# Kernel optimization log

Measured on AMD Instinct MI355X. Metric: run time of the kernel, lower is better.

The kernel has to match this reference:

```python
import jax, jax.numpy as jnp
import numpy as np

B, S, D, H = 4, 1024, 1024, 16
HD = D // H
MAX_DIST, WIN, MAX_SPAN = 512, 256, 512
TEMP_SCALE = 0.01
EPS = 1e-5


def _ln(x, g, b):
    m = x.mean(-1, keepdims=True)
    v = ((x - m) ** 2).mean(-1, keepdims=True)
    return (x - m) * jax.lax.rsqrt(v + EPS) * g + b


def _heads(t):
    b, s, _ = t.shape
    return t.reshape(b, s, H, HD).transpose(0, 2, 1, 3)


def _merge(t):
    b, _, s, _ = t.shape
    return t.transpose(0, 2, 1, 3).reshape(b, s, D)


def _global_attn(x, Wq, bq, Wk, Wv, bv, Wo, bo):
    # MultiheadC with mask tensor passed -> is_causal=True SDPA (default 1/sqrt(HD) scale)
    q = _heads(x @ Wq.T + bq)
    k = _heads(x @ Wk.T)
    v = _heads(x @ Wv.T + bv)
    s = jnp.einsum('bhqd,bhkd->bhqk', q, k) / float(np.sqrt(HD))
    n = x.shape[1]
    causal = jnp.tril(jnp.ones((n, n), bool))
    s = jnp.where(causal, s, jnp.finfo(s.dtype).min)
    w = jax.nn.softmax(s, axis=-1)
    return _merge(jnp.einsum('bhqk,bhkd->bhqd', w, v)) @ Wo.T + bo


def _span_attn(q, k, v, temp):
    # AdaptiveSpan core: softmax(QK^T / temperature * head_dim**-0.25) V
    scale = HD ** -0.25
    qh, kh, vh = _heads(q), _heads(k), _heads(v)
    w = jax.nn.softmax(jnp.einsum('bhqd,bhkd->bhqk', qh, kh) / temp * scale, axis=-1)
    return _merge(jnp.einsum('bhqk,bhkd->bhqd', w, vh))


def _slide_win(local, span_mean, win, span_len, local_max):
    bx, sx, dx = local.shape
    temp = 1.0 + TEMP_SCALE * (1.0 - span_mean)  # sharpen=True branch
    outs = []
    for st in range(0, sx, win):  # static unrolled loop over windows (ragged slices)
        en = min(st + win, sx)
        wlen = en - st
        ks = max(0, st - span_len + win)
        ke = min(st + span_len, sx)
        klen = ke - ks
        eff = min(int(wlen * span_mean), wlen, klen, local_max)
        if eff <= 0:
            outs.append(jnp.zeros((bx, wlen, dx), local.dtype))
            continue
        o = _span_attn(local[:, st:st + eff], local[:, ks:ks + eff], local[:, ks:ks + eff], temp)
        if eff < wlen:
            o = jnp.concatenate([o, jnp.zeros((bx, wlen - eff, dx), local.dtype)], axis=1)
        outs.append(o)
    return jnp.concatenate(outs, axis=1)


def setup_inputs() -> dict:
    key = jax.random.key(0)
    ks = jax.random.split(key, 8)
    qkv_std = 1.0 / float(np.sqrt(HD))
    return {
        'x': jax.random.normal(ks[0], (B, S, D), jnp.float32),
        'ln_a_g': jnp.ones((D,), jnp.float32),
        'ln_a_b': jnp.zeros((D,), jnp.float32),
        'ln_b_g': jnp.ones((D,), jnp.float32),
        'ln_b_b': jnp.zeros((D,), jnp.float32),
        'Wq': jax.random.normal(ks[1], (D, D), jnp.float32) * qkv_std,
        'bq': jnp.zeros((D,), jnp.float32),
        'Wk': jax.random.normal(ks[2], (D, D), jnp.float32) * qkv_std,
        'Wv': jax.random.normal(ks[3], (D, D), jnp.float32) * qkv_std,
        'bv': jnp.zeros((D,), jnp.float32),
        'Wo': jax.random.normal(ks[4], (D, D), jnp.float32) * 0.02,
        'bo': jnp.zeros((D,), jnp.float32),
        'Wp': jax.random.normal(ks[5], (1, D), jnp.float32) * float(np.sqrt(2.0 / (D + 1))),
        'bp': jnp.zeros((1,), jnp.float32),
        'Wproj': jax.random.normal(ks[6], (D, 2 * D), jnp.float32) * 0.02,
        'bproj': jnp.zeros((D,), jnp.float32),
    }


def reference(x, ln_a_g, ln_a_b, ln_b_g, ln_b_b, Wq, bq, Wk, Wv, bv, Wo, bo, Wp, bp, Wproj, bproj):
    local = _ln(x, ln_a_g, ln_a_b)
    globe = _ln(x, ln_b_g, ln_b_b)
    globe_out = _global_attn(globe, Wq, bq, Wk, Wv, bv, Wo, bo)
    # Predictor: sigmoid(Linear(mean over seq))
    base_scale = jax.nn.sigmoid(globe_out.mean(axis=1) @ Wp.T + bp)  # [B, 1]
    span_scale = jnp.clip(base_scale, 0.0, 1.0)  # RL refine factor fixed at 1.0 (deterministic)
    span_mean = float(jnp.mean(span_scale))  # mirrors torch .item() host sync
    win = max(1, int(WIN * span_mean))
    span_len = max(1, int(MAX_SPAN * span_mean))
    local_max = min(MAX_DIST, span_len, win)
    local_out = _slide_win(local, span_mean, win, span_len, local_max)
    combined = jnp.concatenate([local_out, globe_out], axis=-1)
    return combined @ Wproj.T + bproj
```

## Files before the change

### kernel.cpp

```cpp
#include <hip/hip_runtime.h>
#include <math.h>

#define B_ 4
#define S_ 1024
#define D_ 1024
#define H_ 16
#define HD_ 64
#define BSD_ (B_*S_*D_)

using short8 = __attribute__((ext_vector_type(8))) short;
using f32x4  = __attribute__((ext_vector_type(4))) float;

#define MFMA16(a,b,c) __builtin_amdgcn_mfma_f32_16x16x32_bf16((a),(b),(c),0,0,0)

__device__ __forceinline__ ushort f2bf(float f) {
  uint u = __float_as_uint(f);
  return (ushort)((u + 0x7fffu + ((u >> 16) & 1u)) >> 16);
}
__device__ __forceinline__ float bf2f(ushort h) {
  return __uint_as_float(((uint)h) << 16);
}
__device__ __forceinline__ void split8(const float* p, short8* hi, short8* lo) {
  #pragma unroll
  for (int j = 0; j < 8; j++) {
    ushort h = f2bf(p[j]);
    (*hi)[j] = (short)h;
    (*lo)[j] = (short)f2bf(p[j] - bf2f(h));
  }
}
__device__ __forceinline__ void async_load16(const ushort* g, ushort* l) {
  __builtin_amdgcn_global_load_lds(
      (const __attribute__((address_space(1))) unsigned int*)g,
      (__attribute__((address_space(3))) unsigned int*)l, 16, 0, 0);
}

__device__ __forceinline__ float block_reduce_sum_256(float v, float* sbuf) {
  #pragma unroll
  for (int off = 32; off > 0; off >>= 1) v += __shfl_xor(v, off, 64);
  int lane = threadIdx.x & 63, wid = threadIdx.x >> 6;
  __syncthreads();
  if (lane == 0) sbuf[wid] = v;
  __syncthreads();
  return sbuf[0] + sbuf[1] + sbuf[2] + sbuf[3];
}

__global__ __launch_bounds__(256) void ln_kernel(const float* __restrict__ x,
                                                 const float* __restrict__ g,
                                                 const float* __restrict__ bta,
                                                 float* __restrict__ out) {
  __shared__ float sbuf[4];
  const int row = blockIdx.x;
  const float* xr = x + (size_t)row * D_;
  const int t = threadIdx.x;
  float v[4]; float s = 0.f;
  #pragma unroll
  for (int i = 0; i < 4; i++) { v[i] = xr[t + 256*i]; s += v[i]; }
  const float mean = block_reduce_sum_256(s, sbuf) * (1.0f/D_);
  float sq = 0.f;
  #pragma unroll
  for (int i = 0; i < 4; i++) { float d = v[i]-mean; sq += d*d; }
  const float var = block_reduce_sum_256(sq, sbuf) * (1.0f/D_);
  const float r = rsqrtf(var + 1e-5f);
  float* orow = out + (size_t)row * D_;
  #pragma unroll
  for (int i = 0; i < 4; i++) {
    int c = t + 256*i;
    orow[c] = (v[i]-mean)*r*g[c] + bta[c];
  }
}

__global__ __launch_bounds__(256) void ln_split_kernel(const float* __restrict__ x,
                                                       const float* __restrict__ g,
                                                       const float* __restrict__ bta,
                                                       ushort* __restrict__ out) {
  __shared__ float sbuf[4];
  const int row = blockIdx.x;
  const int t = threadIdx.x;
  const int c = t*4;
  const float* xr = x + (size_t)row * D_;
  float4 v = *(const float4*)(xr + c);
  float s = v.x + v.y + v.z + v.w;
  const float mean = block_reduce_sum_256(s, sbuf) * (1.0f/D_);
  float4 dv = make_float4(v.x-mean, v.y-mean, v.z-mean, v.w-mean);
  float sq = dv.x*dv.x + dv.y*dv.y + dv.z*dv.z + dv.w*dv.w;
  const float var = block_reduce_sum_256(sq, sbuf) * (1.0f/D_);
  const float r = rsqrtf(var + 1e-5f);
  float4 gg = *(const float4*)(g + c);
  float4 bb = *(const float4*)(bta + c);
  float n[4];
  n[0] = dv.x*r*gg.x + bb.x; n[1] = dv.y*r*gg.y + bb.y;
  n[2] = dv.z*r*gg.z + bb.z; n[3] = dv.w*r*gg.w + bb.w;
  ushort4 hi, lo;
  hi.x = f2bf(n[0]); hi.y = f2bf(n[1]); hi.z = f2bf(n[2]); hi.w = f2bf(n[3]);
  lo.x = f2bf(n[0]-bf2f(hi.x)); lo.y = f2bf(n[1]-bf2f(hi.y));
  lo.z = f2bf(n[2]-bf2f(hi.z)); lo.w = f2bf(n[3]-bf2f(hi.w));
  ushort* orow = out + (size_t)row*2048;
  *(ushort4*)(orow + c)        = hi;
  *(ushort4*)(orow + 1024 + c) = lo;
}

__global__ __launch_bounds__(256) void split_w3_kernel(const float* __restrict__ Wq,
                                                       const float* __restrict__ Wk,
                                                       const float* __restrict__ Wv,
                                                       const float* __restrict__ bq,
                                                       const float* __restrict__ bv,
                                                       ushort* __restrict__ out,
                                                       float* __restrict__ biascat) {
  const int idx = blockIdx.x*256 + threadIdx.x;
  const int n = idx >> 8;
  const int col4 = (idx & 255) << 2;
  const float* src = (n < 1024) ? (Wq + (size_t)n*1024)
                   : (n < 2048) ? (Wk + (size_t)(n-1024)*1024)
                                : (Wv + (size_t)(n-2048)*1024);
  const float4 a = *(const float4*)(src + col4);
  ushort4 hi, lo;
  hi.x = f2bf(a.x); hi.y = f2bf(a.y); hi.z = f2bf(a.z); hi.w = f2bf(a.w);
  lo.x = f2bf(a.x - bf2f(hi.x)); lo.y = f2bf(a.y - bf2f(hi.y));
  lo.z = f2bf(a.z - bf2f(hi.z)); lo.w = f2bf(a.w - bf2f(hi.w));
  ushort* orow = out + (size_t)n*2048;
  *(ushort4*)(orow + col4)        = hi;
  *(ushort4*)(orow + 1024 + col4) = lo;
  if (idx < 3072)
    biascat[idx] = (idx < 1024) ? bq[idx] : (idx < 2048) ? 0.f : bv[idx-2048];
}

__global__ __launch_bounds__(256) void split_w1_kernel(const float* __restrict__ W,
                                                       ushort* __restrict__ out) {
  const int idx = blockIdx.x*256 + threadIdx.x;
  const int n = idx >> 8;
  const int col4 = (idx & 255) << 2;
  const float4 a = *(const float4*)(W + (size_t)n*1024 + col4);
  ushort4 hi, lo;
  hi.x = f2bf(a.x); hi.y = f2bf(a.y); hi.z = f2bf(a.z); hi.w = f2bf(a.w);
  lo.x = f2bf(a.x - bf2f(hi.x)); lo.y = f2bf(a.y - bf2f(hi.y));
  lo.z = f2bf(a.z - bf2f(hi.z)); lo.w = f2bf(a.w - bf2f(hi.w));
  ushort* orow = out + (size_t)n*2048;
  *(ushort4*)(orow + col4)        = hi;
  *(ushort4*)(orow + 1024 + col4) = lo;
}

__global__ __launch_bounds__(256) void cvt_bf16_kernel(const float* __restrict__ in,
                                                       ushort* __restrict__ out,
                                                       int gprshift, int ostride, int ooff) {
  const int idx = blockIdx.x*256 + threadIdx.x;
  const int row = idx >> gprshift;
  const int col4 = (idx & ((1 << gprshift) - 1)) << 2;
  const int ncols = 4 << gprshift;
  const float4 a = *(const float4*)(in + (size_t)row*ncols + col4);
  ushort4 hi;
  hi.x = f2bf(a.x); hi.y = f2bf(a.y); hi.z = f2bf(a.z); hi.w = f2bf(a.w);
  *(ushort4*)(out + (size_t)row*ostride + ooff + col4) = hi;
}

__global__ __launch_bounds__(256) void mfma_gemm_qkv(
    const ushort* __restrict__ A, const ushort* __restrict__ Bw,
    const float* __restrict__ bias,
    ushort* __restrict__ Qsp, ushort* __restrict__ Ksp,
    ushort* __restrict__ Vth, ushort* __restrict__ Vtl, int Kh) {
  __shared__ __align__(16) ushort smem[17408];
  ushort* Ash = smem;
  ushort* Asl = smem + 4096;
  ushort* Bsh = smem + 8192;
  ushort* Bsl = smem + 12288;
  const int lda = 2*Kh;
  const int tid = threadIdx.x;
  const int bm = blockIdx.y * 128, bn = blockIdx.x * 128;
  const int wave = tid >> 6, lane = tid & 63;
  const int wm = wave >> 1, wn = wave & 1;
  const int lm = lane & 15, q = lane >> 4;
  const int lrow = lane >> 2;
  const int sw = (((lane & 3) ^ ((lane >> 3) & 3)) << 3);

  f32x4 acc[4][4];
  #pragma unroll
  for (int i = 0; i < 4; i++)
    #pragma unroll
    for (int j = 0; j < 4; j++)
      acc[i][j] = (f32x4){0.f,0.f,0.f,0.f};

  const ushort* Agh = A  + (size_t)(bm + wave*32 + lrow)*lda + sw;
  const ushort* Agl = Agh + Kh;
  const ushort* Bgh = Bw + (size_t)(bn + wave*32 + lrow)*lda + sw;
  const ushort* Bgl = Bgh + Kh;
  const size_t r16a = (size_t)16*lda;
  ushort* AhD0 = &Ash[(wave*32)*32];      ushort* AhD1 = &Ash[(wave*32+16)*32];
  ushort* AlD0 = &Asl[(wave*32)*32];      ushort* AlD1 = &Asl[(wave*32+16)*32];
  ushort* BhD0 = &Bsh[(wave*32)*32];      ushort* BhD1 = &Bsh[(wave*32+16)*32];
  ushort* BlD0 = &Bsl[(wave*32)*32];      ushort* BlD1 = &Bsl[(wave*32+16)*32];
  const int rsw  = ((q ^ ((lm >> 1) & 3)) << 3);
  const int aoff = (wm*64 + lm)*32 + rsw;
  const int boff = (wn*64 + lm)*32 + rsw;

  for (int k0 = 0; k0 < Kh; k0 += 32) {
    __syncthreads();
    async_load16(Agh + k0, AhD0);
    async_load16(Agh + r16a + k0, AhD1);
    async_load16(Agl + k0, AlD0);
    async_load16(Agl + r16a + k0, AlD1);
    async_load16(Bgh + k0, BhD0);
    async_load16(Bgh + r16a + k0, BhD1);
    async_load16(Bgl + k0, BlD0);
    async_load16(Bgl + r16a + k0, BlD1);
    __syncthreads();
    short8 ah[4], al[4], bh[4], bl[4];
    #pragma unroll
    for (int mt = 0; mt < 4; mt++) {
      ah[mt] = *(const short8*)&Ash[aoff + mt*512];
      al[mt] = *(const short8*)&Asl[aoff + mt*512];
    }
    #pragma unroll
    for (int nt = 0; nt < 4; nt++) {
      bh[nt] = *(const short8*)&Bsh[boff + nt*512];
      bl[nt] = *(const short8*)&Bsl[boff + nt*512];
    }
    #pragma unroll
    for (int mt = 0; mt < 4; mt++)
      #pragma unroll
      for (int nt = 0; nt < 4; nt++) {
        f32x4 a = acc[mt][nt];
        a = MFMA16(ah[mt], bh[nt], a);
        a = MFMA16(al[mt], bh[nt], a);
        a = MFMA16(ah[mt], bl[nt], a);
        acc[mt][nt] = a;
      }
  }

  const int b = bm >> 10, s0 = bm & 1023;
  if (blockIdx.x < 16) {
    ushort* dst = (blockIdx.x < 8) ? Qsp : Ksp;
    const int h = ((bn + wn*64) >> 6) & 15;
    #pragma unroll
    for (int mt = 0; mt < 4; mt++) {
      #pragma unroll
      for (int nt = 0; nt < 4; nt++) {
        const int n = bn + wn*64 + nt*16 + lm;
        const int d = nt*16 + lm;
        const float bb = bias[n];
        #pragma unroll
        for (int reg = 0; reg < 4; reg++) {
          const int s = s0 + wm*64 + mt*16 + q*4 + reg;
          const float val = acc[mt][nt][reg] + bb;
          const ushort hi = f2bf(val);
          const ushort lo = f2bf(val - bf2f(hi));
          ushort* rp = dst + ((size_t)((b*16 + h)*1024 + s))*128;
          rp[d] = hi; rp[64 + d] = lo;
        }
      }
    }
  } else {
    ushort* Th = smem;
    ushort* Tl = smem + 8704;
    #pragma unroll
    for (int c = 0; c < 2; c++) {
      __syncthreads();
      if (wn == c) {
        #pragma unroll
        for (int mt = 0; mt < 4; mt++)
          #pragma unroll
          for (int nt = 0; nt < 4; nt++) {
            const int nl = nt*16 + lm;
            const float bb = bias[bn + c*64 + nl];
            #pragma unroll
            for (int reg = 0; reg < 4; reg++) {
              const int sl = wm*64 + mt*16 + q*4 + reg;
              const float val = acc[mt][nt][reg] + bb;
              const ushort hi = f2bf(val);
              const ushort lo = f2bf(val - bf2f(hi));
              Th[nl*136 + sl] = hi;
              Tl[nl*136 + sl] = lo;
            }
          }
      }
      __syncthreads();
      const int nl = tid >> 2, s32 = (tid & 3)*32;
      const int h = ((bn - 2048 + c*64) >> 6) & 15;
      const size_t drow = ((size_t)((b*16 + h)*64 + nl))*1024 + s0 + s32;
      #pragma unroll
      for (int j = 0; j < 4; j++) {
        *(short8*)(Vth + drow + j*8) = *(const short8*)&Th[nl*136 + s32 + j*8];
        *(short8*)(Vtl + drow + j*8) = *(const short8*)&Tl[nl*136 + s32 + j*8];
      }
    }
  }
}

__global__ __launch_bounds__(256) void mfma_gemm2(
    const ushort* __restrict__ A, const ushort* __restrict__ Bw,
    const float* __restrict__ bias, float* __restrict__ C,
    int Kh, int ldc, ushort* __restrict__ aux) {
  __shared__ __align__(16) ushort Ash[128*32];
  __shared__ __align__(16) ushort Asl[128*32];
  __shared__ __align__(16) ushort Bsh[128*32];
  __shared__ __align__(16) ushort Bsl[128*32];
  const int lda = 2*Kh;
  const int tid = threadIdx.x;
  const int bm = blockIdx.y * 128, bn = blockIdx.x * 128;
  const int wave = tid >> 6, lane = tid & 63;
  const int wm = wave >> 1, wn = wave & 1;
  const int lm = lane & 15, q = lane >> 4;
  const int lrow = lane >> 2;
  const int sw = (((lane & 3) ^ ((lane >> 3) & 3)) << 3);

  f32x4 acc[4][4];
  #pragma unroll
  for (int i = 0; i < 4; i++)
    #pragma unroll
    for (int j = 0; j < 4; j++)
      acc[i][j] = (f32x4){0.f,0.f,0.f,0.f};

  const ushort* Agh = A  + (size_t)(bm + wave*32 + lrow)*lda + sw;
  const ushort* Agl = Agh + Kh;
  const ushort* Bgh = Bw + (size_t)(bn + wave*32 + lrow)*lda + sw;
  const ushort* Bgl = Bgh + Kh;
  const size_t r16a = (size_t)16*lda;
  ushort* AhD0 = &Ash[(wave*32)*32];      ushort* AhD1 = &Ash[(wave*32+16)*32];
  ushort* AlD0 = &Asl[(wave*32)*32];      ushort* AlD1 = &Asl[(wave*32+16)*32];
  ushort* BhD0 = &Bsh[(wave*32)*32];      ushort* BhD1 = &Bsh[(wave*32+16)*32];
  ushort* BlD0 = &Bsl[(wave*32)*32];      ushort* BlD1 = &Bsl[(wave*32+16)*32];
  const int rsw  = ((q ^ ((lm >> 1) & 3)) << 3);
  const int aoff = (wm*64 + lm)*32 + rsw;
  const int boff = (wn*64 + lm)*32 + rsw;

  for (int k0 = 0; k0 < Kh; k0 += 32) {
    __syncthreads();
    async_load16(Agh + k0, AhD0);
    async_load16(Agh + r16a + k0, AhD1);
    async_load16(Agl + k0, AlD0);
    async_load16(Agl + r16a + k0, AlD1);
    async_load16(Bgh + k0, BhD0);
    async_load16(Bgh + r16a + k0, BhD1);
    async_load16(Bgl + k0, BlD0);
    async_load16(Bgl + r16a + k0, BlD1);
    __syncthreads();
    short8 ah[4], al[4], bh[4], bl[4];
    #pragma unroll
    for (int mt = 0; mt < 4; mt++) {
      ah[mt] = *(const short8*)&Ash[aoff + mt*512];
      al[mt] = *(const short8*)&Asl[aoff + mt*512];
    }
    #pragma unroll
    for (int nt = 0; nt < 4; nt++) {
      bh[nt] = *(const short8*)&Bsh[boff + nt*512];
      bl[nt] = *(const short8*)&Bsl[boff + nt*512];
    }
    #pragma unroll
    for (int mt = 0; mt < 4; mt++)
      #pragma unroll
      for (int nt = 0; nt < 4; nt++) {
        f32x4 a = acc[mt][nt];
        a = MFMA16(ah[mt], bh[nt], a);
        a = MFMA16(al[mt], bh[nt], a);
        a = MFMA16(ah[mt], bl[nt], a);
        acc[mt][nt] = a;
      }
  }

  #pragma unroll
  for (int mt = 0; mt < 4; mt++) {
    #pragma unroll
    for (int nt = 0; nt < 4; nt++) {
      const int n = bn + wn*64 + nt*16 + lm;
      const float bb = bias ? bias[n] : 0.f;
      #pragma unroll
      for (int reg = 0; reg < 4; reg++) {
        const int m = bm + wm*64 + mt*16 + q*4 + reg;
        const float val = acc[mt][nt][reg] + bb;
        C[(size_t)m*ldc + n] = val;
        if (aux) aux[(size_t)m*2048 + 1024 + n] = f2bf(val);
      }
    }
  }
}

__global__ __launch_bounds__(256) void mfma_gemm(
    const ushort* __restrict__ A, const ushort* __restrict__ Bw,
    const float* __restrict__ bias, float* __restrict__ C,
    int K, int ldc) {
  __shared__ __align__(16) ushort As[128*32];
  __shared__ __align__(16) ushort Bs[128*32];
  const int tid = threadIdx.x;
  const int bm = blockIdx.y * 128, bn = blockIdx.x * 128;
  const int wave = tid >> 6, lane = tid & 63;
  const int wm = wave >> 1, wn = wave & 1;
  const int lm = lane & 15, q = lane >> 4;
  const int lrow = lane >> 2;
  const int sw = (((lane & 3) ^ ((lane >> 3) & 3)) << 3);

  f32x4 acc[4][4];
  #pragma unroll
  for (int i = 0; i < 4; i++)
    #pragma unroll
    for (int j = 0; j < 4; j++)
      acc[i][j] = (f32x4){0.f,0.f,0.f,0.f};

  const ushort* Ar0 = A  + (size_t)(bm + wave*32 + lrow)*K + sw;
  const ushort* Br0 = Bw + (size_t)(bn + wave*32 + lrow)*K + sw;
  const size_t r16 = (size_t)16*K;
  ushort* AsD0 = &As[(wave*32)*32];
  ushort* AsD1 = &As[(wave*32 + 16)*32];
  ushort* BsD0 = &Bs[(wave*32)*32];
  ushort* BsD1 = &Bs[(wave*32 + 16)*32];
  const int rsw  = ((q ^ ((lm >> 1) & 3)) << 3);
  const int aoff0 = (wm*64 + lm)*32 + rsw;
  const int boff0 = (wn*64 + lm)*32 + rsw;

  for (int k0 = 0; k0 < K; k0 += 32) {
    __syncthreads();
    async_load16(Ar0 + k0, AsD0);
    async_load16(Ar0 + r16 + k0, AsD1);
    async_load16(Br0 + k0, BsD0);
    async_load16(Br0 + r16 + k0, BsD1);
    __syncthreads();
    short8 af[4], bf[4];
    #pragma unroll
    for (int mt = 0; mt < 4; mt++) af[mt] = *(const short8*)&As[aoff0 + mt*512];
    #pragma unroll
    for (int nt = 0; nt < 4; nt++) bf[nt] = *(const short8*)&Bs[boff0 + nt*512];
    #pragma unroll
    for (int mt = 0; mt < 4; mt++)
      #pragma unroll
      for (int nt = 0; nt < 4; nt++)
        acc[mt][nt] = MFMA16(af[mt], bf[nt], acc[mt][nt]);
  }

  #pragma unroll
  for (int mt = 0; mt < 4; mt++) {
    #pragma unroll
    for (int nt = 0; nt < 4; nt++) {
      const int n = bn + wn*64 + nt*16 + lm;
      const float bb = bias ? bias[n] : 0.f;
      #pragma unroll
      for (int reg = 0; reg < 4; reg++) {
        const int m = bm + wm*64 + mt*16 + q*4 + reg;
        C[(size_t)m*ldc + n] = acc[mt][nt][reg] + bb;
      }
    }
  }
}

__device__ __forceinline__ void attn_unit(
    int qt, int kt, int w, int lm, int q,
    const short8 qh[2], const short8 ql[2],
    const ushort* Kc, const ushort* Vc, float* Pf,
    f32x4 of[4], float mst[4], float lst[4]) {
  f32x4 sS[4];
  #pragma unroll
  for (int nt = 0; nt < 4; nt++) {
    const ushort* kr = &Kc[(nt*16 + lm)*136 + q*8];
    const short8 kh0 = *(const short8*)(kr);
    const short8 kh1 = *(const short8*)(kr + 32);
    const short8 kl0 = *(const short8*)(kr + 64);
    const short8 kl1 = *(const short8*)(kr + 96);
    f32x4 a = (f32x4){0.f,0.f,0.f,0.f};
    a = MFMA16(qh[0], kh0, a);
    a = MFMA16(ql[0], kh0, a);
    a = MFMA16(qh[0], kl0, a);
    a = MFMA16(qh[1], kh1, a);
    a = MFMA16(ql[1], kh1, a);
    a = MFMA16(qh[1], kl1, a);
    sS[nt] = a;
  }
  const int ktbase = kt*64;
  const int qrow0 = qt*64 + w*16 + q*4;
  #pragma unroll
  for (int rm = 0; rm < 4; rm++) {
    const int qrow = qrow0 + rm;
    float v[4];
    #pragma unroll
    for (int nt = 0; nt < 4; nt++) {
      const int kcol = ktbase + nt*16 + lm;
      const float x = sS[nt][rm]*0.125f;
      v[nt] = (kcol <= qrow) ? x : -INFINITY;
    }
    float tm = fmaxf(fmaxf(v[0],v[1]), fmaxf(v[2],v[3]));
    #pragma unroll
    for (int off = 1; off < 16; off <<= 1) tm = fmaxf(tm, __shfl_xor(tm, off, 64));
    const float nm = fmaxf(mst[rm], tm);
    const float alpha = __expf(mst[rm] - nm);
    float ps = 0.f;
    #pragma unroll
    for (int nt = 0; nt < 4; nt++) {
      float p = __expf(v[nt] - nm);
      sS[nt][rm] = p;
      ps += p;
    }
    #pragma unroll
    for (int off = 1; off < 16; off <<= 1) ps += __shfl_xor(ps, off, 64);
    lst[rm] = lst[rm]*alpha + ps;
    mst[rm] = nm;
    #pragma unroll
    for (int nt = 0; nt < 4; nt++) of[nt][rm] *= alpha;
  }
  #pragma unroll
  for (int rm = 0; rm < 4; rm++)
    #pragma unroll
    for (int nt = 0; nt < 4; nt++)
      Pf[(w*16 + q*4 + rm)*66 + nt*16 + lm] = sS[nt][rm];
  short8 ph[2], pl[2];
  {
    const float* prow = &Pf[(w*16 + lm)*66];
    float pv[16];
    *(float4*)&pv[0]  = *(const float4*)(prow + q*8);
    *(float4*)&pv[4]  = *(const float4*)(prow + q*8 + 4);
    *(float4*)&pv[8]  = *(const float4*)(prow + 32 + q*8);
    *(float4*)&pv[12] = *(const float4*)(prow + 32 + q*8 + 4);
    split8(&pv[0], &ph[0], &pl[0]);
    split8(&pv[8], &ph[1], &pl[1]);
  }
  #pragma unroll
  for (int nt = 0; nt < 4; nt++) {
    const ushort* vr = &Vc[(nt*16 + lm)*136 + q*8];
    const short8 vh0 = *(const short8*)(vr);
    const short8 vh1 = *(const short8*)(vr + 32);
    const short8 vl0 = *(const short8*)(vr + 64);
    const short8 vl1 = *(const short8*)(vr + 96);
    f32x4 a = of[nt];
    a = MFMA16(ph[0], vh0, a);
    a = MFMA16(pl[0], vh0, a);
    a = MFMA16(ph[0], vl0, a);
    a = MFMA16(ph[1], vh1, a);
    a = MFMA16(pl[1], vh1, a);
    a = MFMA16(ph[1], vl1, a);
    of[nt] = a;
  }
}

__global__ __launch_bounds__(256) void gattn_mfma(
    const ushort* __restrict__ Qsp, const ushort* __restrict__ Ksp,
    const ushort* __restrict__ Vth, const ushort* __restrict__ Vtl,
    ushort* __restrict__ Aout) {
  __shared__ __align__(16) ushort Kc[64*136];
  __shared__ __align__(16) ushort Vc[64*136];
  __shared__ __align__(16) float  Pf[64*66];
  const int bh = blockIdx.y;
  const int b = bh >> 4, h = bh & 15;
  const int tid = threadIdx.x;
  const int w = tid >> 6, lane = tid & 63;
  const int lm = lane & 15, q = lane >> 4;
  const ushort* Qb_ = Qsp + (size_t)bh * (1024*128);
  const ushort* Kb_ = Ksp + (size_t)bh * (1024*128);
  const ushort* Vhb = Vth + (size_t)bh * (64*1024);
  const ushort* Vlb = Vtl + (size_t)bh * (64*1024);
  const int qtA = 15 - blockIdx.x;
  const int qtB = blockIdx.x;

  short8 qhA[2], qlA[2], qhB[2], qlB[2];
  {
    const ushort* qr = Qb_ + (size_t)(qtA*64 + w*16 + lm)*128 + q*8;
    qhA[0] = *(const short8*)(qr);
    qhA[1] = *(const short8*)(qr + 32);
    qlA[0] = *(const short8*)(qr + 64);
    qlA[1] = *(const short8*)(qr + 96);
    const ushort* qr2 = Qb_ + (size_t)(qtB*64 + w*16 + lm)*128 + q*8;
    qhB[0] = *(const short8*)(qr2);
    qhB[1] = *(const short8*)(qr2 + 32);
    qlB[0] = *(const short8*)(qr2 + 64);
    qlB[1] = *(const short8*)(qr2 + 96);
  }
  f32x4 ofA[4], ofB[4];
  float mstA[4], lstA[4], mstB[4], lstB[4];
  #pragma unroll
  for (int nt = 0; nt < 4; nt++) {
    ofA[nt] = (f32x4){0.f,0.f,0.f,0.f};
    ofB[nt] = (f32x4){0.f,0.f,0.f,0.f};
  }
  #pragma unroll
  for (int rm = 0; rm < 4; rm++) {
    mstA[rm] = -INFINITY; lstA[rm] = 0.f;
    mstB[rm] = -INFINITY; lstB[rm] = 0.f;
  }

  for (int kt = 0; kt <= qtA; ++kt) {
    __syncthreads();
    #pragma unroll
    for (int i = 0; i < 4; i++) {
      const int slot = i*256 + tid;
      const int row = slot >> 4, c8 = slot & 15;
      *(float4*)&Kc[row*136 + c8*8] =
          *(const float4*)(Kb_ + (size_t)(kt*64 + row)*128 + c8*8);
      const ushort* vsrc = ((c8 < 8) ? Vhb : Vlb) + (size_t)row*1024 + kt*64 + (c8&7)*8;
      *(float4*)&Vc[row*136 + c8*8] = *(const float4*)vsrc;
    }
    __syncthreads();
    attn_unit(qtA, kt, w, lm, q, qhA, qlA, Kc, Vc, Pf, ofA, mstA, lstA);
    if (kt <= qtB)
      attn_unit(qtB, kt, w, lm, q, qhB, qlB, Kc, Vc, Pf, ofB, mstB, lstB);
  }

  #pragma unroll
  for (int rm = 0; rm < 4; rm++) {
    const float invA = 1.0f / lstA[rm];
    const int sA = qtA*64 + w*16 + q*4 + rm;
    ushort* arow = Aout + ((size_t)(b*1024 + sA))*2048 + h*64;
    #pragma unroll
    for (int nt = 0; nt < 4; nt++) {
      const float val = ofA[nt][rm] * invA;
      const ushort hi = f2bf(val);
      arow[nt*16 + lm] = hi;
      arow[1024 + nt*16 + lm] = f2bf(val - bf2f(hi));
    }
    const float invB = 1.0f / lstB[rm];
    const int sB = qtB*64 + w*16 + q*4 + rm;
    ushort* brow = Aout + ((size_t)(b*1024 + sB))*2048 + h*64;
    #pragma unroll
    for (int nt = 0; nt < 4; nt++) {
      const float val = ofB[nt][rm] * invB;
      const ushort hi = f2bf(val);
      brow[nt*16 + lm] = hi;
      brow[1024 + nt*16 + lm] = f2bf(val - bf2f(hi));
    }
  }
}

__global__ __launch_bounds__(256) void seqmean1_kernel(const float* __restrict__ g,
                                                       float* __restrict__ part) {
  const int d = blockIdx.x*256 + threadIdx.x;
  const int sc = blockIdx.y;
  const int b = blockIdx.z;
  const float* p = g + ((size_t)b*S_ + sc*128)*D_ + d;
  float s = 0.f;
  #pragma unroll 4
  for (int i = 0; i < 128; i++) s += p[(size_t)i*D_];
  part[((size_t)(b*8 + sc))*D_ + d] = s;
}
__global__ __launch_bounds__(256) void seqmean2_kernel(const float* __restrict__ part,
                                                       float* __restrict__ mbd) {
  const int d = blockIdx.x*256 + threadIdx.x;
  const int b = blockIdx.y;
  float s = 0.f;
  #pragma unroll
  for (int i = 0; i < 8; i++) s += part[((size_t)(b*8 + i))*D_ + d];
  mbd[b*D_ + d] = s * (1.0f/S_);
}

__global__ __launch_bounds__(256) void predictor_kernel(
    const float* __restrict__ mbd, const float* __restrict__ Wp,
    const float* __restrict__ bp, float* __restrict__ fpar, int* __restrict__ ipar) {
  __shared__ float sbuf[4];
  __shared__ float sdots[4];
  const int tid = threadIdx.x;
  for (int b = 0; b < 4; b++) {
    float psum = 0.f;
    for (int d = tid; d < D_; d += 256) psum += mbd[b*D_ + d]*Wp[d];
    float tot = block_reduce_sum_256(psum, sbuf);
    if (tid == 0) sdots[b] = tot;
  }
  __syncthreads();
  if (tid == 0) {
    float smv = 0.f;
    for (int b = 0; b < 4; b++) {
      float z = sdots[b] + bp[0];
      smv += 1.0f/(1.0f + expf(-z));
    }
    smv *= 0.25f;
    int win = max(1, (int)(256.0f*smv));
    int span_len = max(1, (int)(512.0f*smv));
    int local_max = min(512, min(span_len, win));
    float temp = 1.0f + 0.01f*(1.0f - smv);
    int n_win = (S_ + win - 1)/win;
    fpar[0] = smv; fpar[1] = temp;
    ipar[0] = win; ipar[1] = span_len; ipar[2] = local_max; ipar[3] = n_win;
  }
}

#define LDP 68
__global__ __launch_bounds__(256) void lattn_kernel(
    const float* __restrict__ Lc, ushort* __restrict__ Out,
    const int* __restrict__ ip, const float* __restrict__ fpp) {
  __shared__ __align__(16) float Qs[HD_][LDP];
  __shared__ __align__(16) float KPs[64][LDP];
  __shared__ __align__(16) float Vs[64][LDP];
  const int n_win = ip[3];
  const int win = ip[0], span_len = ip[1], local_max = ip[2];
  const float sm = fpp[0], temp = fpp[1];
  const int bh = blockIdx.y;
  const int b = bh >> 4, h = bh & 15;
  const int tid = threadIdx.x;
  const int tx = tid & 15, ty = tid >> 4;
  const float sc = 0.35355339059327373f / temp;
  for (int w = blockIdx.x; w < n_win; w += gridDim.x) {
    const int st = w * win;
    const int en = min(st + win, S_); const int wlen = en - st;
    const int ks = max(0, st - span_len + win);
    const int ke = min(st + span_len, S_); const int klen = ke - ks;
    int eff = (int)((double)wlen * (double)sm);
    eff = min(min(eff, wlen), min(klen, local_max));
    if (eff > 0) {
      const int nt = (eff + 63) >> 6;
      for (int qt = 0; qt < nt; ++qt) {
        const int qn = min(64, eff - qt*64);
        __syncthreads();
        #pragma unroll
        for (int c = 0; c < 4; c++) {
          int f = tid + c*256;
          int r = f >> 4;
          int dc = (f & 15) << 2;
          float4 q4 = make_float4(0.f,0.f,0.f,0.f);
          if (r < qn) q4 = *(const float4*)(Lc + ((size_t)(b*S_ + st + qt*64 + r)) * D_ + h*HD_ + dc);
          Qs[dc+0][r]=q4.x; Qs[dc+1][r]=q4.y; Qs[dc+2][r]=q4.z; Qs[dc+3][r]=q4.w;
        }
        float o[4][4] = {{0.f,0.f,0.f,0.f},{0.f,0.f,0.f,0.f},{0.f,0.f,0.f,0.f},{0.f,0.f,0.f,0.f}};
        float mrow[4], lrow[4];
        #pragma unroll
        for (int i=0;i<4;i++){ mrow[i] = -INFINITY; lrow[i] = 0.f; }
        for (int kt = 0; kt < nt; ++kt) {
          const int kn = min(64, eff - kt*64);
          __syncthreads();
          #pragma unroll
          for (int c = 0; c < 4; c++) {
            int f = tid + c*256;
            int r = f >> 4;
            int dc = (f & 15) << 2;
            float4 k4 = make_float4(0.f,0.f,0.f,0.f);
            if (r < kn) k4 = *(const float4*)(Lc + ((size_t)(b*S_ + ks + kt*64 + r)) * D_ + h*HD_ + dc);
            KPs[dc+0][r]=k4.x; KPs[dc+1][r]=k4.y; KPs[dc+2][r]=k4.z; KPs[dc+3][r]=k4.w;
            *(float4*)&Vs[r][dc] = k4;
          }
          __syncthreads();
          float s[4][4] = {{0.f,0.f,0.f,0.f},{0.f,0.f,0.f,0.f},{0.f,0.f,0.f,0.f},{0.f,0.f,0.f,0.f}};
          #pragma unroll 8
          for (int d = 0; d < HD_; ++d) {
            const float4 a  = *(const float4*)&Qs[d][ty*4];
            const float4 bb = *(const float4*)&KPs[d][tx*4];
            const float av[4]={a.x,a.y,a.z,a.w};
            const float bv[4]={bb.x,bb.y,bb.z,bb.w};
            #pragma unroll
            for (int i=0;i<4;i++)
              #pragma unroll
              for (int j=0;j<4;j++)
                s[i][j] += av[i]*bv[j];
          }
          #pragma unroll
          for (int i=0;i<4;i++) {
            #pragma unroll
            for (int j=0;j<4;j++) {
              float lg = s[i][j]*sc;
              if (kt*64 + tx*4 + j >= eff) lg = -INFINITY;
              s[i][j] = lg;
            }
          }
          #pragma unroll
          for (int i=0;i<4;i++) {
            float tm = fmaxf(fmaxf(s[i][0],s[i][1]), fmaxf(s[i][2],s[i][3]));
            #pragma unroll
            for (int off=1; off<16; off<<=1) tm = fmaxf(tm, __shfl_xor(tm, off, 64));
            const float nm = fmaxf(mrow[i], tm);
            const float alpha = __expf(mrow[i]-nm);
            float ps = 0.f;
            #pragma unroll
            for (int j=0;j<4;j++){ float p = __expf(s[i][j]-nm); s[i][j]=p; ps += p; }
            #pragma unroll
            for (int off=1; off<16; off<<=1) ps += __shfl_xor(ps, off, 64);
            lrow[i] = lrow[i]*alpha + ps;
            mrow[i] = nm;
            #pragma unroll
            for (int j=0;j<4;j++) o[i][j] *= alpha;
          }
          __syncthreads();
          #pragma unroll
          for (int i=0;i<4;i++)
            #pragma unroll
            for (int j=0;j<4;j++)
              KPs[tx*4+j][ty*4+i] = s[i][j];
          __syncthreads();
          #pragma unroll 8
          for (int kk = 0; kk < 64; ++kk) {
            const float4 a  = *(const float4*)&KPs[kk][ty*4];
            const float4 bb = *(const float4*)&Vs[kk][tx*4];
            const float av[4]={a.x,a.y,a.z,a.w};
            const float bv[4]={bb.x,bb.y,bb.z,bb.w};
            #pragma unroll
            for (int i=0;i<4;i++)
              #pragma unroll
              for (int j=0;j<4;j++)
                o[i][j] += av[i]*bv[j];
          }
        }
        #pragma unroll
        for (int i=0;i<4;i++){
          const int r = ty*4 + i;
          if (r < qn) {
            const float inv = 1.0f / lrow[i];
            ushort4 ov;
            ov.x = f2bf(o[i][0]*inv); ov.y = f2bf(o[i][1]*inv);
            ov.z = f2bf(o[i][2]*inv); ov.w = f2bf(o[i][3]*inv);
            *(ushort4*)(Out + ((size_t)(b*S_ + st + qt*64 + r)) * 2048 + h*HD_ + tx*4) = ov;
          }
        }
      }
    }
    const ushort4 z = {0,0,0,0};
    for (int r = max(eff, 0) + ty; r < wlen; r += 16)
      *(ushort4*)(Out + ((size_t)(b*S_ + st + r)) * 2048 + h*HD_ + tx*4) = z;
  }
}

extern "C" void kernel_launch(void* const* d_in, const int* in_sizes, int n_in,
                              void* d_out, int out_size, void* d_ws, size_t ws_size,
                              hipStream_t stream) {
  const float* x      = (const float*)d_in[0];
  const float* ln_a_g = (const float*)d_in[1];
  const float* ln_a_b = (const float*)d_in[2];
  const float* ln_b_g = (const float*)d_in[3];
  const float* ln_b_b = (const float*)d_in[4];
  const float* Wq     = (const float*)d_in[5];
  const float* bq     = (const float*)d_in[6];
  const float* Wk     = (const float*)d_in[7];
  const float* Wv     = (const float*)d_in[8];
  const float* bv     = (const float*)d_in[9];
  const float* Wo     = (const float*)d_in[10];
  const float* bo     = (const float*)d_in[11];
  const float* Wp     = (const float*)d_in[12];
  const float* bp     = (const float*)d_in[13];
  const float* Wproj  = (const float*)d_in[14];
  const float* bproj  = (const float*)d_in[15];
  float* out = (float*)d_out;
  float* ws  = (float*)d_ws;
  ushort* wsu = (ushort*)d_ws;

  ushort* Qsp = wsu;
  ushort* Ksp = wsu + 8388608;
  ushort* Vth = wsu + 16777216;
  ushort* Vtl = wsu + 20971520;
  float* glo  = ws + 16777216;
  float* loc  = ws + 20971520;
  float* biascat = ws + 25165824;
  float* mbd  = biascat + 4096;
  float* fpar = mbd + 4096;
  int*   ipar = (int*)(fpar + 8);
  ushort* Acat  = (ushort*)(ws + 25182208);
  ushort* Bqkv  = Acat + 12582912;
  ushort* Bo    = Bqkv + 9437184;
  float*  part = (float*)Acat;
  ushort* A3  = wsu;
  ushort* B3  = wsu + 8388608;

  const dim3 blk(256);

  ln_split_kernel<<<dim3(B_*S_), blk, 0, stream>>>(x, ln_b_g, ln_b_b, Acat);
  split_w3_kernel<<<dim3(3072), blk, 0, stream>>>(Wq, Wk, Wv, bq, bv, Bqkv, biascat);
  mfma_gemm_qkv<<<dim3(24, 32), blk, 0, stream>>>(Acat, Bqkv, biascat,
                                                  Qsp, Ksp, Vth, Vtl, 1024);
  gattn_mfma<<<dim3(8, 64), blk, 0, stream>>>(Qsp, Ksp, Vth, Vtl, Acat);
  split_w1_kernel<<<dim3(1024), blk, 0, stream>>>(Wo, Bo);
  mfma_gemm2<<<dim3(8, 32), blk, 0, stream>>>(Acat, Bo, bo, glo, 1024, 1024, A3);
  seqmean1_kernel<<<dim3(4, 8, B_), blk, 0, stream>>>(glo, part);
  seqmean2_kernel<<<dim3(4, B_), blk, 0, stream>>>(part, mbd);
  predictor_kernel<<<dim3(1), blk, 0, stream>>>(mbd, Wp, bp, fpar, ipar);
  ln_kernel<<<dim3(B_*S_), blk, 0, stream>>>(x, ln_a_g, ln_a_b, loc);
  lattn_kernel<<<dim3(64, B_*H_), blk, 0, stream>>>(loc, A3, ipar, fpar);
  cvt_bf16_kernel<<<dim3(2048), blk, 0, stream>>>(Wproj, B3, 9, 2048, 0);
  mfma_gemm<<<dim3(8, 32), blk, 0, stream>>>(A3, B3, bproj, out, 2048, 1024);
}
```

Baseline: 480.0 us.

## Fuse prep kernels into one launch and halve GEMM M-tile for more blocks

Merges the two layernorms, the weight hi/lo splits and the Wproj bf16 conversion into a single prep_kernel, with blockIdx ranges selecting each role. This removes several launches and lets that independent work overlap. The Wo and final projection GEMMs change from 128x128 to 64x128 tiles, doubling the grid to 512 blocks for better CU occupancy, at the cost of more B-tile reloads. B3 moves to a new workspace offset so it is not overwritten now that it is produced early.

```diff
diff --git a/kernel.cpp b/kernel.cpp
--- a/kernel.cpp
+++ b/kernel.cpp
@@ -44,112 +44,90 @@
   return sbuf[0] + sbuf[1] + sbuf[2] + sbuf[3];
 }
 
-__global__ __launch_bounds__(256) void ln_kernel(const float* __restrict__ x,
-                                                 const float* __restrict__ g,
-                                                 const float* __restrict__ bta,
-                                                 float* __restrict__ out) {
-  __shared__ float sbuf[4];
-  const int row = blockIdx.x;
-  const float* xr = x + (size_t)row * D_;
-  const int t = threadIdx.x;
-  float v[4]; float s = 0.f;
-  #pragma unroll
-  for (int i = 0; i < 4; i++) { v[i] = xr[t + 256*i]; s += v[i]; }
-  const float mean = block_reduce_sum_256(s, sbuf) * (1.0f/D_);
-  float sq = 0.f;
-  #pragma unroll
-  for (int i = 0; i < 4; i++) { float d = v[i]-mean; sq += d*d; }
-  const float var = block_reduce_sum_256(sq, sbuf) * (1.0f/D_);
-  const float r = rsqrtf(var + 1e-5f);
-  float* orow = out + (size_t)row * D_;
-  #pragma unroll
-  for (int i = 0; i < 4; i++) {
-    int c = t + 256*i;
-    orow[c] = (v[i]-mean)*r*g[c] + bta[c];
-  }
-}
-
-__global__ __launch_bounds__(256) void ln_split_kernel(const float* __restrict__ x,
-                                                       const float* __restrict__ g,
-                                                       const float* __restrict__ bta,
-                                                       ushort* __restrict__ out) {
-  __shared__ float sbuf[4];
-  const int row = blockIdx.x;
-  const int t = threadIdx.x;
-  const int c = t*4;
-  const float* xr = x + (size_t)row * D_;
-  float4 v = *(const float4*)(xr + c);
-  float s = v.x + v.y + v.z + v.w;
-  const float mean = block_reduce_sum_256(s, sbuf) * (1.0f/D_);
-  float4 dv = make_float4(v.x-mean, v.y-mean, v.z-mean, v.w-mean);
-  float sq = dv.x*dv.x + dv.y*dv.y + dv.z*dv.z + dv.w*dv.w;
-  const float var = block_reduce_sum_256(sq, sbuf) * (1.0f/D_);
-  const float r = rsqrtf(var + 1e-5f);
-  float4 gg = *(const float4*)(g + c);
-  float4 bb = *(const float4*)(bta + c);
-  float n[4];
-  n[0] = dv.x*r*gg.x + bb.x; n[1] = dv.y*r*gg.y + bb.y;
-  n[2] = dv.z*r*gg.z + bb.z; n[3] = dv.w*r*gg.w + bb.w;
-  ushort4 hi, lo;
-  hi.x = f2bf(n[0]); hi.y = f2bf(n[1]); hi.z = f2bf(n[2]); hi.w = f2bf(n[3]);
-  lo.x = f2bf(n[0]-bf2f(hi.x)); lo.y = f2bf(n[1]-bf2f(hi.y));
-  lo.z = f2bf(n[2]-bf2f(hi.z)); lo.w = f2bf(n[3]-bf2f(hi.w));
-  ushort* orow = out + (size_t)row*2048;
-  *(ushort4*)(orow + c)        = hi;
-  *(ushort4*)(orow + 1024 + c) = lo;
-}
-
-__global__ __launch_bounds__(256) void split_w3_kernel(const float* __restrict__ Wq,
-                                                       const float* __restrict__ Wk,
-                                                       const float* __restrict__ Wv,
-                                                       const float* __restrict__ bq,
-                                                       const float* __restrict__ bv,
-                                                       ushort* __restrict__ out,
-                                                       float* __restrict__ biascat) {
-  const int idx = blockIdx.x*256 + threadIdx.x;
-  const int n = idx >> 8;
-  const int col4 = (idx & 255) << 2;
-  const float* src = (n < 1024) ? (Wq + (size_t)n*1024)
-                   : (n < 2048) ? (Wk + (size_t)(n-1024)*1024)
-                                : (Wv + (size_t)(n-2048)*1024);
-  const float4 a = *(const float4*)(src + col4);
+__device__ __forceinline__ void split4_store(const float4 a, ushort* orow, int c, int stride) {
   ushort4 hi, lo;
   hi.x = f2bf(a.x); hi.y = f2bf(a.y); hi.z = f2bf(a.z); hi.w = f2bf(a.w);
   lo.x = f2bf(a.x - bf2f(hi.x)); lo.y = f2bf(a.y - bf2f(hi.y));
   lo.z = f2bf(a.z - bf2f(hi.z)); lo.w = f2bf(a.w - bf2f(hi.w));
-  ushort* orow = out + (size_t)n*2048;
-  *(ushort4*)(orow + col4)        = hi;
-  *(ushort4*)(orow + 1024 + col4) = lo;
-  if (idx < 3072)
-    biascat[idx] = (idx < 1024) ? bq[idx] : (idx < 2048) ? 0.f : bv[idx-2048];
-}
-
-__global__ __launch_bounds__(256) void split_w1_kernel(const float* __restrict__ W,
-                                                       ushort* __restrict__ out) {
-  const int idx = blockIdx.x*256 + threadIdx.x;
-  const int n = idx >> 8;
-  const int col4 = (idx & 255) << 2;
-  const float4 a = *(const float4*)(W + (size_t)n*1024 + col4);
-  ushort4 hi, lo;
-  hi.x = f2bf(a.x); hi.y = f2bf(a.y); hi.z = f2bf(a.z); hi.w = f2bf(a.w);
-  lo.x = f2bf(a.x - bf2f(hi.x)); lo.y = f2bf(a.y - bf2f(hi.y));
-  lo.z = f2bf(a.z - bf2f(hi.z)); lo.w = f2bf(a.w - bf2f(hi.w));
-  ushort* orow = out + (size_t)n*2048;
-  *(ushort4*)(orow + col4)        = hi;
-  *(ushort4*)(orow + 1024 + col4) = lo;
-}
-
-__global__ __launch_bounds__(256) void cvt_bf16_kernel(const float* __restrict__ in,
-                                                       ushort* __restrict__ out,
-                                                       int gprshift, int ostride, int ooff) {
-  const int idx = blockIdx.x*256 + threadIdx.x;
-  const int row = idx >> gprshift;
-  const int col4 = (idx & ((1 << gprshift) - 1)) << 2;
-  const int ncols = 4 << gprshift;
-  const float4 a = *(const float4*)(in + (size_t)row*ncols + col4);
-  ushort4 hi;
-  hi.x = f2bf(a.x); hi.y = f2bf(a.y); hi.z = f2bf(a.z); hi.w = f2bf(a.w);
-  *(ushort4*)(out + (size_t)row*ostride + ooff + col4) = hi;
+  *(ushort4*)(orow + c)          = hi;
+  *(ushort4*)(orow + stride + c) = lo;
+}
+
+__global__ __launch_bounds__(256) void prep_kernel(
+    const float* __restrict__ x,
+    const float* __restrict__ ln_a_g, const float* __restrict__ ln_a_b,
+    const float* __restrict__ ln_b_g, const float* __restrict__ ln_b_b,
+    const float* __restrict__ Wq, const float* __restrict__ Wk,
+    const float* __restrict__ Wv, const float* __restrict__ bq,
+    const float* __restrict__ bv, const float* __restrict__ Wo,
+    const float* __restrict__ Wproj,
+    ushort* __restrict__ Acat, ushort* __restrict__ Bqkv,
+    float* __restrict__ biascat, float* __restrict__ loc,
+    ushort* __restrict__ B3, ushort* __restrict__ Bo) {
+  __shared__ float sbuf[4];
+  const int bx = blockIdx.x;
+  const int t = threadIdx.x;
+  if (bx < 4096) {
+    const int row = bx;
+    const int c = t*4;
+    const float* xr = x + (size_t)row * D_;
+    float4 v = *(const float4*)(xr + c);
+    float s = v.x + v.y + v.z + v.w;
+    const float mean = block_reduce_sum_256(s, sbuf) * (1.0f/D_);
+    float4 dv = make_float4(v.x-mean, v.y-mean, v.z-mean, v.w-mean);
+    float sq = dv.x*dv.x + dv.y*dv.y + dv.z*dv.z + dv.w*dv.w;
+    const float var = block_reduce_sum_256(sq, sbuf) * (1.0f/D_);
+    const float r = rsqrtf(var + 1e-5f);
+    float4 gg = *(const float4*)(ln_b_g + c);
+    float4 bb = *(const float4*)(ln_b_b + c);
+    float4 n;
+    n.x = dv.x*r*gg.x + bb.x; n.y = dv.y*r*gg.y + bb.y;
+    n.z = dv.z*r*gg.z + bb.z; n.w = dv.w*r*gg.w + bb.w;
+    split4_store(n, Acat + (size_t)row*2048, c, 1024);
+  } else if (bx < 7168) {
+    const int idx = (bx - 4096)*256 + t;
+    const int n = idx >> 8;
+    const int col4 = (idx & 255) << 2;
+    const float* src = (n < 1024) ? (Wq + (size_t)n*1024)
+                     : (n < 2048) ? (Wk + (size_t)(n-1024)*1024)
+                                  : (Wv + (size_t)(n-2048)*1024);
+    const float4 a = *(const float4*)(src + col4);
+    split4_store(a, Bqkv + (size_t)n*2048, col4, 1024);
+    if (idx < 3072)
+      biascat[idx] = (idx < 1024) ? bq[idx] : (idx < 2048) ? 0.f : bv[idx-2048];
+  } else if (bx < 11264) {
+    const int row = bx - 7168;
+    const float* xr = x + (size_t)row * D_;
+    float v[4]; float s = 0.f;
+    #pragma unroll
+    for (int i = 0; i < 4; i++) { v[i] = xr[t + 256*i]; s += v[i]; }
+    const float mean = block_reduce_sum_256(s, sbuf) * (1.0f/D_);
+    float sq = 0.f;
+    #pragma unroll
+    for (int i = 0; i < 4; i++) { float d = v[i]-mean; sq += d*d; }
+    const float var = block_reduce_sum_256(sq, sbuf) * (1.0f/D_);
+    const float r = rsqrtf(var + 1e-5f);
+    float* orow = loc + (size_t)row * D_;
+    #pragma unroll
+    for (int i = 0; i < 4; i++) {
+      int c = t + 256*i;
+      orow[c] = (v[i]-mean)*r*ln_a_g[c] + ln_a_b[c];
+    }
+  } else if (bx < 13312) {
+    const int idx = (bx - 11264)*256 + t;
+    const int row = idx >> 9;
+    const int col4 = (idx & 511) << 2;
+    const float4 a = *(const float4*)(Wproj + (size_t)row*2048 + col4);
+    ushort4 hi;
+    hi.x = f2bf(a.x); hi.y = f2bf(a.y); hi.z = f2bf(a.z); hi.w = f2bf(a.w);
+    *(ushort4*)(B3 + (size_t)row*2048 + col4) = hi;
+  } else {
+    const int idx = (bx - 13312)*256 + t;
+    const int n = idx >> 8;
+    const int col4 = (idx & 255) << 2;
+    const float4 a = *(const float4*)(Wo + (size_t)n*1024 + col4);
+    split4_store(a, Bo + (size_t)n*2048, col4, 1024);
+  }
 }
 
 __global__ __launch_bounds__(256) void mfma_gemm_qkv(
@@ -288,65 +266,61 @@
     const ushort* __restrict__ A, const ushort* __restrict__ Bw,
     const float* __restrict__ bias, float* __restrict__ C,
     int Kh, int ldc, ushort* __restrict__ aux) {
-  __shared__ __align__(16) ushort Ash[128*32];
-  __shared__ __align__(16) ushort Asl[128*32];
+  __shared__ __align__(16) ushort Ash[64*32];
+  __shared__ __align__(16) ushort Asl[64*32];
   __shared__ __align__(16) ushort Bsh[128*32];
   __shared__ __align__(16) ushort Bsl[128*32];
   const int lda = 2*Kh;
   const int tid = threadIdx.x;
-  const int bm = blockIdx.y * 128, bn = blockIdx.x * 128;
+  const int bm = blockIdx.y * 64, bn = blockIdx.x * 128;
   const int wave = tid >> 6, lane = tid & 63;
-  const int wm = wave >> 1, wn = wave & 1;
   const int lm = lane & 15, q = lane >> 4;
   const int lrow = lane >> 2;
   const int sw = (((lane & 3) ^ ((lane >> 3) & 3)) << 3);
 
-  f32x4 acc[4][4];
+  f32x4 acc[4][2];
   #pragma unroll
   for (int i = 0; i < 4; i++)
     #pragma unroll
-    for (int j = 0; j < 4; j++)
+    for (int j = 0; j < 2; j++)
       acc[i][j] = (f32x4){0.f,0.f,0.f,0.f};
 
-  const ushort* Agh = A  + (size_t)(bm + wave*32 + lrow)*lda + sw;
-  const ushort* Agl = Agh + Kh;
-  const ushort* Bgh = Bw + (size_t)(bn + wave*32 + lrow)*lda + sw;
-  const ushort* Bgl = Bgh + Kh;
-  const size_t r16a = (size_t)16*lda;
-  ushort* AhD0 = &Ash[(wave*32)*32];      ushort* AhD1 = &Ash[(wave*32+16)*32];
-  ushort* AlD0 = &Asl[(wave*32)*32];      ushort* AlD1 = &Asl[(wave*32+16)*32];
-  ushort* BhD0 = &Bsh[(wave*32)*32];      ushort* BhD1 = &Bsh[(wave*32+16)*32];
-  ushort* BlD0 = &Bsl[(wave*32)*32];      ushort* BlD1 = &Bsl[(wave*32+16)*32];
-  const int rsw  = ((q ^ ((lm >> 1) & 3)) << 3);
-  const int aoff = (wm*64 + lm)*32 + rsw;
-  const int boff = (wn*64 + lm)*32 + rsw;
+  const ushort* gsrc[6];
+  ushort* ldst[6];
+  #pragma unroll
+  for (int i = 0; i < 6; i++) {
+    const int s = wave*6 + i;
+    const ushort* gp; ushort* lp;
+    if (s < 4)       { gp = A  + (size_t)(bm + s*16 + lrow)*lda + sw;           lp = &Ash[(s*16)*32]; }
+    else if (s < 8)  { gp = A  + (size_t)(bm + (s-4)*16 + lrow)*lda + Kh + sw;  lp = &Asl[((s-4)*16)*32]; }
+    else if (s < 16) { gp = Bw + (size_t)(bn + (s-8)*16 + lrow)*lda + sw;       lp = &Bsh[((s-8)*16)*32]; }
+    else             { gp = Bw + (size_t)(bn + (s-16)*16 + lrow)*lda + Kh + sw; lp = &Bsl[((s-16)*16)*32]; }
+    gsrc[i] = gp; ldst[i] = lp;
+  }
+  const int rsw = ((q ^ ((lm >> 1) & 3)) << 3);
+  const int aoff = lm*32 + rsw;
+  const int boff = (wave*32 + lm)*32 + rsw;
 
   for (int k0 = 0; k0 < Kh; k0 += 32) {
     __syncthreads();
-    async_load16(Agh + k0, AhD0);
-    async_load16(Agh + r16a + k0, AhD1);
-    async_load16(Agl + k0, AlD0);
-    async_load16(Agl + r16a + k0, AlD1);
-    async_load16(Bgh + k0, BhD0);
-    async_load16(Bgh + r16a + k0, BhD1);
-    async_load16(Bgl + k0, BlD0);
-    async_load16(Bgl + r16a + k0, BlD1);
+    #pragma unroll
+    for (int i = 0; i < 6; i++) async_load16(gsrc[i] + k0, ldst[i]);
     __syncthreads();
-    short8 ah[4], al[4], bh[4], bl[4];
+    short8 ah[4], al[4], bh[2], bl[2];
     #pragma unroll
     for (int mt = 0; mt < 4; mt++) {
       ah[mt] = *(const short8*)&Ash[aoff + mt*512];
       al[mt] = *(const short8*)&Asl[aoff + mt*512];
     }
     #pragma unroll
-    for (int nt = 0; nt < 4; nt++) {
+    for (int nt = 0; nt < 2; nt++) {
       bh[nt] = *(const short8*)&Bsh[boff + nt*512];
       bl[nt] = *(const short8*)&Bsl[boff + nt*512];
     }
     #pragma unroll
     for (int mt = 0; mt < 4; mt++)
       #pragma unroll
-      for (int nt = 0; nt < 4; nt++) {
+      for (int nt = 0; nt < 2; nt++) {
         f32x4 a = acc[mt][nt];
         a = MFMA16(ah[mt], bh[nt], a);
         a = MFMA16(al[mt], bh[nt], a);
@@ -358,12 +332,12 @@
   #pragma unroll
   for (int mt = 0; mt < 4; mt++) {
     #pragma unroll
-    for (int nt = 0; nt < 4; nt++) {
-      const int n = bn + wn*64 + nt*16 + lm;
+    for (int nt = 0; nt < 2; nt++) {
+      const int n = bn + wave*32 + nt*16 + lm;
       const float bb = bias ? bias[n] : 0.f;
       #pragma unroll
       for (int reg = 0; reg < 4; reg++) {
-        const int m = bm + wm*64 + mt*16 + q*4 + reg;
+        const int m = bm + mt*16 + q*4 + reg;
         const float val = acc[mt][nt][reg] + bb;
         C[(size_t)m*ldc + n] = val;
         if (aux) aux[(size_t)m*2048 + 1024 + n] = f2bf(val);
@@ -376,62 +350,62 @@
     const ushort* __restrict__ A, const ushort* __restrict__ Bw,
     const float* __restrict__ bias, float* __restrict__ C,
     int K, int ldc) {
-  __shared__ __align__(16) ushort As[128*32];
+  __shared__ __align__(16) ushort As[64*32];
   __shared__ __align__(16) ushort Bs[128*32];
   const int tid = threadIdx.x;
-  const int bm = blockIdx.y * 128, bn = blockIdx.x * 128;
+  const int bm = blockIdx.y * 64, bn = blockIdx.x * 128;
   const int wave = tid >> 6, lane = tid & 63;
-  const int wm = wave >> 1, wn = wave & 1;
   const int lm = lane & 15, q = lane >> 4;
   const int lrow = lane >> 2;
   const int sw = (((lane & 3) ^ ((lane >> 3) & 3)) << 3);
 
-  f32x4 acc[4][4];
+  f32x4 acc[4][2];
   #pragma unroll
   for (int i = 0; i < 4; i++)
     #pragma unroll
-    for (int j = 0; j < 4; j++)
+    for (int j = 0; j < 2; j++)
       acc[i][j] = (f32x4){0.f,0.f,0.f,0.f};
 
-  const ushort* Ar0 = A  + (size_t)(bm + wave*32 + lrow)*K + sw;
-  const ushort* Br0 = Bw + (size_t)(bn + wave*32 + lrow)*K + sw;
-  const size_t r16 = (size_t)16*K;
-  ushort* AsD0 = &As[(wave*32)*32];
-  ushort* AsD1 = &As[(wave*32 + 16)*32];
-  ushort* BsD0 = &Bs[(wave*32)*32];
-  ushort* BsD1 = &Bs[(wave*32 + 16)*32];
-  const int rsw  = ((q ^ ((lm >> 1) & 3)) << 3);
-  const int aoff0 = (wm*64 + lm)*32 + rsw;
-  const int boff0 = (wn*64 + lm)*32 + rsw;
+  const ushort* gsrc[3];
+  ushort* ldst[3];
+  #pragma unroll
+  for (int i = 0; i < 3; i++) {
+    const int s = wave*3 + i;
+    const ushort* gp; ushort* lp;
+    if (s < 4) { gp = A  + (size_t)(bm + s*16 + lrow)*K + sw;     lp = &As[(s*16)*32]; }
+    else       { gp = Bw + (size_t)(bn + (s-4)*16 + lrow)*K + sw; lp = &Bs[((s-4)*16)*32]; }
+    gsrc[i] = gp; ldst[i] = lp;
+  }
+  const int rsw = ((q ^ ((lm >> 1) & 3)) << 3);
+  const int aoff = lm*32 + rsw;
+  const int boff = (wave*32 + lm)*32 + rsw;
 
   for (int k0 = 0; k0 < K; k0 += 32) {
     __syncthreads();
-    async_load16(Ar0 + k0, AsD0);
-    async_load16(Ar0 + r16 + k0, AsD1);
-    async_load16(Br0 + k0, BsD0);
-    async_load16(Br0 + r16 + k0, BsD1);
+    #pragma unroll
+    for (int i = 0; i < 3; i++) async_load16(gsrc[i] + k0, ldst[i]);
     __syncthreads();
-    short8 af[4], bf[4];
-    #pragma unroll
-    for (int mt = 0; mt < 4; mt++) af[mt] = *(const short8*)&As[aoff0 + mt*512];
-    #pragma unroll
-    for (int nt = 0; nt < 4; nt++) bf[nt] = *(const short8*)&Bs[boff0 + nt*512];
+    short8 af[4], bf[2];
+    #pragma unroll
+    for (int mt = 0; mt < 4; mt++) af[mt] = *(const short8*)&As[aoff + mt*512];
+    #pragma unroll
+    for (int nt = 0; nt < 2; nt++) bf[nt] = *(const short8*)&Bs[boff + nt*512];
     #pragma unroll
     for (int mt = 0; mt < 4; mt++)
       #pragma unroll
-      for (int nt = 0; nt < 4; nt++)
+      for (int nt = 0; nt < 2; nt++)
         acc[mt][nt] = MFMA16(af[mt], bf[nt], acc[mt][nt]);
   }
 
   #pragma unroll
   for (int mt = 0; mt < 4; mt++) {
     #pragma unroll
-    for (int nt = 0; nt < 4; nt++) {
-      const int n = bn + wn*64 + nt*16 + lm;
+    for (int nt = 0; nt < 2; nt++) {
+      const int n = bn + wave*32 + nt*16 + lm;
       const float bb = bias ? bias[n] : 0.f;
       #pragma unroll
       for (int reg = 0; reg < 4; reg++) {
-        const int m = bm + wm*64 + mt*16 + q*4 + reg;
+        const int m = bm + mt*16 + q*4 + reg;
         C[(size_t)m*ldc + n] = acc[mt][nt][reg] + bb;
       }
     }
@@ -822,6 +796,7 @@
   ushort* Ksp = wsu + 8388608;
   ushort* Vth = wsu + 16777216;
   ushort* Vtl = wsu + 20971520;
+  ushort* B3  = (ushort*)(ws + 12582912);
   float* glo  = ws + 16777216;
   float* loc  = ws + 20971520;
   float* biascat = ws + 25165824;
@@ -833,22 +808,19 @@
   ushort* Bo    = Bqkv + 9437184;
   float*  part = (float*)Acat;
   ushort* A3  = wsu;
-  ushort* B3  = wsu + 8388608;
 
   const dim3 blk(256);
 
-  ln_split_kernel<<<dim3(B_*S_), blk, 0, stream>>>(x, ln_b_g, ln_b_b, Acat);
-  split_w3_kernel<<<dim3(3072), blk, 0, stream>>>(Wq, Wk, Wv, bq, bv, Bqkv, biascat);
+  prep_kernel<<<dim3(14336), blk, 0, stream>>>(
+      x, ln_a_g, ln_a_b, ln_b_g, ln_b_b, Wq, Wk, Wv, bq, bv, Wo, Wproj,
+      Acat, Bqkv, biascat, loc, B3, Bo);
   mfma_gemm_qkv<<<dim3(24, 32), blk, 0, stream>>>(Acat, Bqkv, biascat,
                                                   Qsp, Ksp, Vth, Vtl, 1024);
   gattn_mfma<<<dim3(8, 64), blk, 0, stream>>>(Qsp, Ksp, Vth, Vtl, Acat);
-  split_w1_kernel<<<dim3(1024), blk, 0, stream>>>(Wo, Bo);
-  mfma_gemm2<<<dim3(8, 32), blk, 0, stream>>>(Acat, Bo, bo, glo, 1024, 1024, A3);
+  mfma_gemm2<<<dim3(8, 64), blk, 0, stream>>>(Acat, Bo, bo, glo, 1024, 1024, A3);
   seqmean1_kernel<<<dim3(4, 8, B_), blk, 0, stream>>>(glo, part);
   seqmean2_kernel<<<dim3(4, B_), blk, 0, stream>>>(part, mbd);
   predictor_kernel<<<dim3(1), blk, 0, stream>>>(mbd, Wp, bp, fpar, ipar);
-  ln_kernel<<<dim3(B_*S_), blk, 0, stream>>>(x, ln_a_g, ln_a_b, loc);
   lattn_kernel<<<dim3(64, B_*H_), blk, 0, stream>>>(loc, A3, ipar, fpar);
-  cvt_bf16_kernel<<<dim3(2048), blk, 0, stream>>>(Wproj, B3, 9, 2048, 0);
-  mfma_gemm<<<dim3(8, 32), blk, 0, stream>>>(A3, B3, bproj, out, 2048, 1024);
-}
+  mfma_gemm<<<dim3(8, 64), blk, 0, stream>>>(A3, B3, bproj, out, 2048, 1024);
+}
```

After: 453.4 us. 5.5% less time.
